# Optimization experiments

Measured on AMD Instinct MI355X. Metric: run time of the kernel, lower is better.

## Reference

```python
import jax, jax.numpy as jnp
import numpy as np

DIM = 768
HEADS = 12
HIDDEN = 4 * DIM
B, N = 8, 1024
EPS = 1e-5


def setup_inputs() -> dict:
    key = jax.random.key(0)
    ks = jax.random.split(key, 8)
    s = 0.02
    return {
        "x": jax.random.normal(ks[0], (B, N, DIM), dtype=jnp.float32),
        "ln1_g": jnp.ones((DIM,), jnp.float32),
        "ln1_b": jnp.zeros((DIM,), jnp.float32),
        "qkv_w": jax.random.normal(ks[1], (3 * DIM, DIM), jnp.float32) * s,
        "proj_w": jax.random.normal(ks[2], (DIM, DIM), jnp.float32) * s,
        "proj_b": jnp.zeros((DIM,), jnp.float32),
        "ln2_g": jnp.ones((DIM,), jnp.float32),
        "ln2_b": jnp.zeros((DIM,), jnp.float32),
        "fc1_w": jax.random.normal(ks[3], (HIDDEN, DIM), jnp.float32) * s,
        "fc1_b": jnp.zeros((HIDDEN,), jnp.float32),
        "fc2_w": jax.random.normal(ks[4], (DIM, HIDDEN), jnp.float32) * s,
        "fc2_b": jnp.zeros((DIM,), jnp.float32),
    }


def _layernorm(x, g, b):
    mu = jnp.mean(x, axis=-1, keepdims=True)
    var = jnp.mean(jnp.square(x - mu), axis=-1, keepdims=True)
    return (x - mu) * jax.lax.rsqrt(var + EPS) * g + b


def reference(x, ln1_g, ln1_b, qkv_w, proj_w, proj_b, ln2_g, ln2_b, fc1_w, fc1_b, fc2_w, fc2_b):
    Bn, Nn, C = x.shape
    H = HEADS
    D = C // H
    scale = D ** -0.5

    # --- attention branch ---
    h = _layernorm(x, ln1_g, ln1_b)
    qkv = h @ qkv_w.T                      # [B,N,3C] (qkv_bias=False)
    qkv = qkv.reshape(Bn, Nn, 3, H, D)
    q = qkv[:, :, 0].transpose(0, 2, 1, 3)  # [B,H,N,D]
    k = qkv[:, :, 1].transpose(0, 2, 1, 3)
    v = qkv[:, :, 2].transpose(0, 2, 1, 3)
    attn = jnp.einsum('bhnd,bhmd->bhnm', q, k) * scale  # [B,H,N,N]
    attn = jax.nn.softmax(attn, axis=-1)
    ctx = jnp.einsum('bhnm,bhmd->bhnd', attn, v)         # [B,H,N,D]
    ctx = ctx.transpose(0, 2, 1, 3).reshape(Bn, Nn, C)
    x = x + ctx @ proj_w.T + proj_b

    # --- MLP branch ---
    h = _layernorm(x, ln2_g, ln2_b)
    h = jax.nn.gelu(h @ fc1_w.T + fc1_b, approximate=False)
    return x + h @ fc2_w.T + fc2_b
```

## Files before the change

kernel.cpp:

```cpp
#include <hip/hip_runtime.h>
#include <cstdint>

typedef __attribute__((ext_vector_type(8))) short short8;
typedef __attribute__((ext_vector_type(4))) float f32x4;
typedef unsigned short u16t;

__device__ __forceinline__ u16t f2bf(float f) {
  uint32_t u = __float_as_uint(f);
  u += 0x7fffu + ((u >> 16) & 1u);
  return (u16t)(u >> 16);
}

__device__ __forceinline__ void gload_lds16(const void* g, void* l) {
  __builtin_amdgcn_global_load_lds(
      (const __attribute__((address_space(1))) void*)g,
      (__attribute__((address_space(3))) void*)l, 16, 0, 0);
}

__global__ __launch_bounds__(256) void cvt_bf16_kernel(const float* __restrict__ in,
                                                       u16t* __restrict__ out, int n8) {
  int i = blockIdx.x * 256 + threadIdx.x;
  if (i >= n8) return;
  const float4* p = (const float4*)in + (size_t)i * 2;
  float4 a = p[0], b = p[1];
  union { short8 v; u16t e[8]; } r;
  r.e[0] = f2bf(a.x); r.e[1] = f2bf(a.y); r.e[2] = f2bf(a.z); r.e[3] = f2bf(a.w);
  r.e[4] = f2bf(b.x); r.e[5] = f2bf(b.y); r.e[6] = f2bf(b.z); r.e[7] = f2bf(b.w);
  *((short8*)out + i) = r.v;
}

__global__ __launch_bounds__(256) void ln_kernel(const float* __restrict__ x,
                                                 const float* __restrict__ g,
                                                 const float* __restrict__ b,
                                                 u16t* __restrict__ out) {
  int row = blockIdx.x, tid = threadIdx.x;
  int wave = tid >> 6, lane = tid & 63;
  const float* xr = x + (size_t)row * 768;
  float v0 = xr[tid], v1 = xr[tid + 256], v2 = xr[tid + 512];
  float s = v0 + v1 + v2;
  float q = v0 * v0 + v1 * v1 + v2 * v2;
#pragma unroll
  for (int m = 32; m >= 1; m >>= 1) {
    s += __shfl_xor(s, m, 64);
    q += __shfl_xor(q, m, 64);
  }
  __shared__ float red[8];
  if (lane == 0) { red[wave] = s; red[4 + wave] = q; }
  __syncthreads();
  s = red[0] + red[1] + red[2] + red[3];
  q = red[4] + red[5] + red[6] + red[7];
  float mu = s * (1.0f / 768.0f);
  float var = q * (1.0f / 768.0f) - mu * mu;
  float rs = rsqrtf(var + 1e-5f);
  u16t* orow = out + (size_t)row * 768;
  orow[tid]       = f2bf((v0 - mu) * rs * g[tid]       + b[tid]);
  orow[tid + 256] = f2bf((v1 - mu) * rs * g[tid + 256] + b[tid + 256]);
  orow[tid + 512] = f2bf((v2 - mu) * rs * g[tid + 512] + b[tid + 512]);
}

template <int EPI, int BM>
__global__ __launch_bounds__(256, 2) void gemm_bt(const u16t* __restrict__ A,
                                                  const u16t* __restrict__ W,
                                                  void* __restrict__ Cout,
                                                  const float* __restrict__ bias,
                                                  const float* __restrict__ res,
                                                  int M, int N, int K) {
  __shared__ __align__(16) u16t As[BM * 64];
  __shared__ __align__(16) u16t Bs[128 * 64];
  constexpr int MF = BM / 32;
  int tid = threadIdx.x;
  int wave = tid >> 6, lane = tid & 63;
  int wr = wave >> 1, wc = wave & 1;
  int bm = blockIdx.y * BM;
  int bn = blockIdx.x * 128;
  f32x4 acc[MF][4] = {};

  int lr = lane >> 3;
  int lc = lane & 7;
  int srcslot = lc ^ lr;
  const u16t* Abase = A + (size_t)(bm + lr) * K + srcslot * 8;
  const u16t* Wbase = W + (size_t)(bn + lr) * K + srcslot * 8;

  for (int kt = 0; kt < K; kt += 64) {
    __syncthreads();
#pragma unroll
    for (int i = 0; i < BM / 32; i++) {
      int chunk = wave * (BM / 32) + i;
      gload_lds16(Abase + (size_t)(chunk * 8) * K + kt, (void*)(As + chunk * 512));
    }
#pragma unroll
    for (int i = 0; i < 4; i++) {
      int chunk = wave * 4 + i;
      gload_lds16(Wbase + (size_t)(chunk * 8) * K + kt, (void*)(Bs + chunk * 512));
    }
    __syncthreads();

    short8 af[MF][2], bfr[4][2];
#pragma unroll
    for (int m = 0; m < MF; m++) {
      int row = wr * (BM / 2) + m * 16 + (lane & 15);
#pragma unroll
      for (int s = 0; s < 2; s++) {
        int slot = s * 4 + (lane >> 4);
        af[m][s] = *(const short8*)(As + row * 64 + ((slot ^ (row & 7)) * 8));
      }
    }
#pragma unroll
    for (int n = 0; n < 4; n++) {
      int row = wc * 64 + n * 16 + (lane & 15);
#pragma unroll
      for (int s = 0; s < 2; s++) {
        int slot = s * 4 + (lane >> 4);
        bfr[n][s] = *(const short8*)(Bs + row * 64 + ((slot ^ (row & 7)) * 8));
      }
    }
    __builtin_amdgcn_s_setprio(1);
#pragma unroll
    for (int m = 0; m < MF; m++)
#pragma unroll
      for (int n = 0; n < 4; n++) {
        acc[m][n] = __builtin_amdgcn_mfma_f32_16x16x32_bf16(af[m][0], bfr[n][0], acc[m][n], 0, 0, 0);
        acc[m][n] = __builtin_amdgcn_mfma_f32_16x16x32_bf16(af[m][1], bfr[n][1], acc[m][n], 0, 0, 0);
      }
    __builtin_amdgcn_s_setprio(0);
  }

#pragma unroll
  for (int m = 0; m < MF; m++) {
#pragma unroll
    for (int n = 0; n < 4; n++) {
      int r0 = bm + wr * (BM / 2) + m * 16 + (lane >> 4) * 4;
      int c = bn + wc * 64 + n * 16 + (lane & 15);
#pragma unroll
      for (int i = 0; i < 4; i++) {
        int r = r0 + i;
        float v = acc[m][n][i];
        if constexpr (EPI == 0) {
          ((u16t*)Cout)[(size_t)r * N + c] = f2bf(v);
        } else if constexpr (EPI == 1) {
          ((float*)Cout)[(size_t)r * N + c] = v + bias[c] + res[(size_t)r * N + c];
        } else {
          v += bias[c];
          float gl = 0.5f * v * (1.0f + erff(v * 0.70710678118f));
          ((u16t*)Cout)[(size_t)r * N + c] = f2bf(gl);
        }
      }
    }
  }
}

__global__ __launch_bounds__(256, 2) void attn_kernel(const u16t* __restrict__ qkv,
                                                      u16t* __restrict__ ctx) {
  __shared__ __align__(16) u16t Ks[2][64 * 64];
  __shared__ __align__(16) u16t Vt[2][64 * 72];
  __shared__ __align__(16) u16t Ps[4][16 * 72];
  int tid = threadIdx.x;
  int wave = tid >> 6, lane = tid & 63;
  int b = blockIdx.x / 12, h = blockIdx.x % 12;
  int qt = blockIdx.y * 64;
  const u16t* base = qkv + (size_t)b * 1024 * 2304 + h * 64;

  int qrow = qt + wave * 16 + (lane & 15);
  const u16t* qp = base + (size_t)qrow * 2304 + (lane >> 4) * 8;
  short8 aq0 = *(const short8*)qp;
  short8 aq1 = *(const short8*)(qp + 32);

  const u16t* kbase = base + 768;
  const u16t* vbase = base + 1536;
  int lr = lane >> 3, lc = lane & 7;
  const u16t* kst = kbase + (size_t)lr * 2304 + ((lc ^ lr) * 8);
  const u16t* vst = vbase + (size_t)lane * 2304 + wave * 16;

  float m_i[4] = {-1e30f, -1e30f, -1e30f, -1e30f};
  float l_i[4] = {0.f, 0.f, 0.f, 0.f};
  f32x4 o[4] = {};
  const float scale = 0.125f;
  u16t* Pw = Ps[wave];

  union { uint4 u; u16t e[8]; } v0u, v1u;

  auto loadV = [&](int kt) {
    const u16t* vp = vst + (size_t)kt * 2304;
    v0u.u = *(const uint4*)vp;
    v1u.u = *(const uint4*)(vp + 8);
  };
  auto stageK = [&](int kt, int buf) {
#pragma unroll
    for (int i = 0; i < 2; i++) {
      int chunk = wave * 2 + i;
      gload_lds16(kst + (size_t)(kt + chunk * 8) * 2304, (void*)(Ks[buf] + chunk * 512));
    }
  };
  auto writeV = [&](int buf) {
#pragma unroll
    for (int j = 0; j < 8; j++) Vt[buf][(wave * 16 + j) * 72 + lane] = v0u.e[j];
#pragma unroll
    for (int j = 0; j < 8; j++) Vt[buf][(wave * 16 + 8 + j) * 72 + lane] = v1u.e[j];
  };

  loadV(0);
  stageK(0, 0);
  writeV(0);
  __syncthreads();

  for (int t = 0; t < 16; ++t) {
    int buf = t & 1;
    if (t < 15) {
      loadV((t + 1) * 64);
      stageK((t + 1) * 64, buf ^ 1);
    }

    const u16t* Kb = Ks[buf];
    f32x4 s[4] = {};
    __builtin_amdgcn_s_setprio(1);
#pragma unroll
    for (int n = 0; n < 4; n++) {
      int row = n * 16 + (lane & 15);
      int s0 = (lane >> 4);
      short8 bk0 = *(const short8*)(Kb + row * 64 + ((s0 ^ (row & 7)) * 8));
      short8 bk1 = *(const short8*)(Kb + row * 64 + (((s0 + 4) ^ (row & 7)) * 8));
      s[n] = __builtin_amdgcn_mfma_f32_16x16x32_bf16(aq0, bk0, s[n], 0, 0, 0);
      s[n] = __builtin_amdgcn_mfma_f32_16x16x32_bf16(aq1, bk1, s[n], 0, 0, 0);
    }
    __builtin_amdgcn_s_setprio(0);

    float alpha[4];
#pragma unroll
    for (int i = 0; i < 4; i++) {
      float mt = fmaxf(fmaxf(s[0][i], s[1][i]), fmaxf(s[2][i], s[3][i]));
      mt = fmaxf(mt, __shfl_xor(mt, 1, 64));
      mt = fmaxf(mt, __shfl_xor(mt, 2, 64));
      mt = fmaxf(mt, __shfl_xor(mt, 4, 64));
      mt = fmaxf(mt, __shfl_xor(mt, 8, 64));
      float mnew = fmaxf(m_i[i], mt * scale);
      alpha[i] = __expf(m_i[i] - mnew);
      m_i[i] = mnew;
    }
    float rsum[4] = {0.f, 0.f, 0.f, 0.f};
#pragma unroll
    for (int n = 0; n < 4; n++)
#pragma unroll
      for (int i = 0; i < 4; i++) {
        float p = __expf(s[n][i] * scale - m_i[i]);
        s[n][i] = p;
        rsum[i] += p;
      }
#pragma unroll
    for (int i = 0; i < 4; i++) {
      rsum[i] += __shfl_xor(rsum[i], 1, 64);
      rsum[i] += __shfl_xor(rsum[i], 2, 64);
      rsum[i] += __shfl_xor(rsum[i], 4, 64);
      rsum[i] += __shfl_xor(rsum[i], 8, 64);
      l_i[i] = l_i[i] * alpha[i] + rsum[i];
    }
#pragma unroll
    for (int n = 0; n < 4; n++)
#pragma unroll
      for (int i = 0; i < 4; i++)
        Pw[((lane >> 4) * 4 + i) * 72 + n * 16 + (lane & 15)] = f2bf(s[n][i]);
#pragma unroll
    for (int nd = 0; nd < 4; nd++)
#pragma unroll
      for (int i = 0; i < 4; i++) o[nd][i] *= alpha[i];
    const u16t* Vb = Vt[buf];
    __builtin_amdgcn_s_setprio(1);
#pragma unroll
    for (int st = 0; st < 2; st++) {
      short8 ap = *(const short8*)(Pw + (lane & 15) * 72 + st * 32 + (lane >> 4) * 8);
#pragma unroll
      for (int nd = 0; nd < 4; nd++) {
        short8 bv = *(const short8*)(Vb + (nd * 16 + (lane & 15)) * 72 + st * 32 + (lane >> 4) * 8);
        o[nd] = __builtin_amdgcn_mfma_f32_16x16x32_bf16(ap, bv, o[nd], 0, 0, 0);
      }
    }
    __builtin_amdgcn_s_setprio(0);

    if (t < 15) writeV(buf ^ 1);
    __syncthreads();
  }

#pragma unroll
  for (int i = 0; i < 4; i++) l_i[i] = 1.0f / l_i[i];
  int q0 = qt + wave * 16 + (lane >> 4) * 4;
#pragma unroll
  for (int i = 0; i < 4; i++) {
    u16t* crow = ctx + (size_t)(b * 1024 + q0 + i) * 768 + h * 64;
#pragma unroll
    for (int nd = 0; nd < 4; nd++)
      crow[nd * 16 + (lane & 15)] = f2bf(o[nd][i] * l_i[i]);
  }
}

extern "C" void kernel_launch(void* const* d_in, const int* in_sizes, int n_in,
                              void* d_out, int out_size, void* d_ws, size_t ws_size,
                              hipStream_t stream) {
  const float* x      = (const float*)d_in[0];
  const float* ln1_g  = (const float*)d_in[1];
  const float* ln1_b  = (const float*)d_in[2];
  const float* qkv_w  = (const float*)d_in[3];
  const float* proj_w = (const float*)d_in[4];
  const float* proj_b = (const float*)d_in[5];
  const float* ln2_g  = (const float*)d_in[6];
  const float* ln2_b  = (const float*)d_in[7];
  const float* fc1_w  = (const float*)d_in[8];
  const float* fc1_b  = (const float*)d_in[9];
  const float* fc2_w  = (const float*)d_in[10];
  const float* fc2_b  = (const float*)d_in[11];

  char* ws = (char*)d_ws;
  u16t* h1   = (u16t*)(ws + 0);
  u16t* qkvb = (u16t*)(ws + 12582912);
  u16t* ctx  = (u16t*)(ws + 50331648);
  float* x2  = (float*)(ws + 62914560);
  u16t* hid  = (u16t*)(ws + 88080384);
  u16t* wq   = (u16t*)(ws + 138412032);
  u16t* wp   = (u16t*)(ws + 141950976);
  u16t* w1   = (u16t*)(ws + 143130624);
  u16t* w2   = (u16t*)(ws + 147849216);
  float* out = (float*)d_out;

  cvt_bf16_kernel<<<864, 256, 0, stream>>>(qkv_w, wq, 221184);
  cvt_bf16_kernel<<<288, 256, 0, stream>>>(proj_w, wp, 73728);
  cvt_bf16_kernel<<<1152, 256, 0, stream>>>(fc1_w, w1, 294912);
  cvt_bf16_kernel<<<1152, 256, 0, stream>>>(fc2_w, w2, 294912);

  ln_kernel<<<8192, 256, 0, stream>>>(x, ln1_g, ln1_b, h1);
  gemm_bt<0, 128><<<dim3(18, 64), 256, 0, stream>>>(h1, wq, qkvb, nullptr, nullptr, 8192, 2304, 768);
  attn_kernel<<<dim3(96, 16), 256, 0, stream>>>(qkvb, ctx);
  gemm_bt<1, 64><<<dim3(6, 128), 256, 0, stream>>>(ctx, wp, x2, proj_b, x, 8192, 768, 768);
  ln_kernel<<<8192, 256, 0, stream>>>(x2, ln2_g, ln2_b, h1);
  gemm_bt<2, 128><<<dim3(24, 64), 256, 0, stream>>>(h1, w1, hid, fc1_b, nullptr, 8192, 3072, 768);
  gemm_bt<1, 64><<<dim3(6, 128), 256, 0, stream>>>(hid, w2, out, fc2_b, x2, 8192, 768, 3072);
}
```

Baseline: 305.9 us.

## Pre-transpose V and restructure attention to load K/V fragments from global

```diff
diff --git a/kernel.cpp b/kernel.cpp
--- a/kernel.cpp
+++ b/kernel.cpp
@@ -9,6 +9,12 @@
   uint32_t u = __float_as_uint(f);
   u += 0x7fffu + ((u >> 16) & 1u);
   return (u16t)(u >> 16);
+}
+
+__device__ __forceinline__ uint32_t cvtpk(float lo, float hi) {
+  uint32_t r;
+  asm("v_cvt_pk_bf16_f32 %0, %1, %2" : "=v"(r) : "v"(lo), "v"(hi));
+  return r;
 }
 
 __device__ __forceinline__ void gload_lds16(const void* g, void* l) {
@@ -149,145 +155,182 @@
   }
 }
 
-__global__ __launch_bounds__(256, 2) void attn_kernel(const u16t* __restrict__ qkv,
+__global__ __launch_bounds__(256) void vtrans_kernel(const u16t* __restrict__ qkv,
+                                                     u16t* __restrict__ vt) {
+  __shared__ u16t T[64][66];
+  int h = blockIdx.x % 12, bb = blockIdx.x / 12, kt = blockIdx.y * 64;
+  int t = threadIdx.x;
+  int r = t >> 2, dc = t & 3;
+  const u16t* src = qkv + (size_t)(bb * 1024 + kt + r) * 2304 + 1536 + h * 64 + dc * 16;
+  union { uint4 u[2]; u16t e[16]; uint32_t w[8]; } buf;
+  buf.u[0] = *(const uint4*)src;
+  buf.u[1] = *(const uint4*)(src + 8);
+#pragma unroll
+  for (int j = 0; j < 8; j++)
+    *(uint32_t*)&T[r][dc * 16 + 2 * j] = buf.w[j];
+  __syncthreads();
+  int d = t >> 2, kc = t & 3;
+  union { uint4 u[2]; u16t e[16]; } o;
+#pragma unroll
+  for (int j = 0; j < 16; j++) o.e[j] = T[kc * 16 + j][d];
+  u16t* dst = vt + ((size_t)blockIdx.x * 64 + d) * 1024 + kt + kc * 16;
+  *(uint4*)dst = o.u[0];
+  *(uint4*)(dst + 8) = o.u[1];
+}
+
+__global__ __launch_bounds__(256, 3) void attn_kernel(const u16t* __restrict__ qkv,
+                                                      const u16t* __restrict__ vt,
                                                       u16t* __restrict__ ctx) {
-  __shared__ __align__(16) u16t Ks[2][64 * 64];
-  __shared__ __align__(16) u16t Vt[2][64 * 72];
-  __shared__ __align__(16) u16t Ps[4][16 * 72];
+  __shared__ __align__(16) u16t Plds[4][32 * 72];
   int tid = threadIdx.x;
   int wave = tid >> 6, lane = tid & 63;
-  int b = blockIdx.x / 12, h = blockIdx.x % 12;
-  int qt = blockIdx.y * 64;
+  int q = lane & 15, g = lane >> 4;
+
+  int bid = blockIdx.x;
+  int xcd = bid & 7, j = bid >> 3;
+  int head = xcd + 8 * (j >> 3);
+  int qt = (j & 7) * 128 + wave * 32;
+  int b = head / 12, h = head % 12;
+
   const u16t* base = qkv + (size_t)b * 1024 * 2304 + h * 64;
-
-  int qrow = qt + wave * 16 + (lane & 15);
-  const u16t* qp = base + (size_t)qrow * 2304 + (lane >> 4) * 8;
-  short8 aq0 = *(const short8*)qp;
-  short8 aq1 = *(const short8*)(qp + 32);
-
   const u16t* kbase = base + 768;
-  const u16t* vbase = base + 1536;
-  int lr = lane >> 3, lc = lane & 7;
-  const u16t* kst = kbase + (size_t)lr * 2304 + ((lc ^ lr) * 8);
-  const u16t* vst = vbase + (size_t)lane * 2304 + wave * 16;
-
-  float m_i[4] = {-1e30f, -1e30f, -1e30f, -1e30f};
-  float l_i[4] = {0.f, 0.f, 0.f, 0.f};
-  f32x4 o[4] = {};
-  const float scale = 0.125f;
-  u16t* Pw = Ps[wave];
-
-  union { uint4 u; u16t e[8]; } v0u, v1u;
-
-  auto loadV = [&](int kt) {
-    const u16t* vp = vst + (size_t)kt * 2304;
-    v0u.u = *(const uint4*)vp;
-    v1u.u = *(const uint4*)(vp + 8);
-  };
-  auto stageK = [&](int kt, int buf) {
-#pragma unroll
-    for (int i = 0; i < 2; i++) {
-      int chunk = wave * 2 + i;
-      gload_lds16(kst + (size_t)(kt + chunk * 8) * 2304, (void*)(Ks[buf] + chunk * 512));
-    }
-  };
-  auto writeV = [&](int buf) {
-#pragma unroll
-    for (int j = 0; j < 8; j++) Vt[buf][(wave * 16 + j) * 72 + lane] = v0u.e[j];
-#pragma unroll
-    for (int j = 0; j < 8; j++) Vt[buf][(wave * 16 + 8 + j) * 72 + lane] = v1u.e[j];
-  };
-
-  loadV(0);
-  stageK(0, 0);
-  writeV(0);
-  __syncthreads();
-
-  for (int t = 0; t < 16; ++t) {
-    int buf = t & 1;
-    if (t < 15) {
-      loadV((t + 1) * 64);
-      stageK((t + 1) * 64, buf ^ 1);
-    }
-
-    const u16t* Kb = Ks[buf];
-    f32x4 s[4] = {};
+  const u16t* vtb = vt + (size_t)head * 64 * 1024;
+
+  short8 qf[2][2];
+#pragma unroll
+  for (int hf = 0; hf < 2; hf++)
+#pragma unroll
+    for (int hh = 0; hh < 2; hh++)
+      qf[hf][hh] = *(const short8*)(base + (size_t)(qt + hf * 16 + q) * 2304 + hh * 32 + g * 8);
+
+  float mA = -1e30f, mB = -1e30f, lA = 0.f, lB = 0.f;
+  f32x4 oA[4] = {}, oB[4] = {};
+  u16t* Pw = Plds[wave];
+
+  for (int kt = 0; kt < 1024; kt += 64) {
+    short8 kf[4][2], vf[4][2];
+#pragma unroll
+    for (int n = 0; n < 4; n++)
+#pragma unroll
+      for (int hh = 0; hh < 2; hh++)
+        kf[n][hh] = *(const short8*)(kbase + (size_t)(kt + n * 16 + q) * 2304 + hh * 32 + g * 8);
+#pragma unroll
+    for (int n = 0; n < 4; n++)
+#pragma unroll
+      for (int hh = 0; hh < 2; hh++)
+        vf[n][hh] = *(const short8*)(vtb + (size_t)(n * 16 + q) * 1024 + kt + hh * 32 + g * 8);
+
+    f32x4 sA[4] = {}, sB[4] = {};
     __builtin_amdgcn_s_setprio(1);
 #pragma unroll
     for (int n = 0; n < 4; n++) {
-      int row = n * 16 + (lane & 15);
-      int s0 = (lane >> 4);
-      short8 bk0 = *(const short8*)(Kb + row * 64 + ((s0 ^ (row & 7)) * 8));
-      short8 bk1 = *(const short8*)(Kb + row * 64 + (((s0 + 4) ^ (row & 7)) * 8));
-      s[n] = __builtin_amdgcn_mfma_f32_16x16x32_bf16(aq0, bk0, s[n], 0, 0, 0);
-      s[n] = __builtin_amdgcn_mfma_f32_16x16x32_bf16(aq1, bk1, s[n], 0, 0, 0);
+      sA[n] = __builtin_amdgcn_mfma_f32_16x16x32_bf16(kf[n][0], qf[0][0], sA[n], 0, 0, 0);
+      sA[n] = __builtin_amdgcn_mfma_f32_16x16x32_bf16(kf[n][1], qf[0][1], sA[n], 0, 0, 0);
+      sB[n] = __builtin_amdgcn_mfma_f32_16x16x32_bf16(kf[n][0], qf[1][0], sB[n], 0, 0, 0);
+      sB[n] = __builtin_amdgcn_mfma_f32_16x16x32_bf16(kf[n][1], qf[1][1], sB[n], 0, 0, 0);
     }
     __builtin_amdgcn_s_setprio(0);
 
-    float alpha[4];
-#pragma unroll
-    for (int i = 0; i < 4; i++) {
-      float mt = fmaxf(fmaxf(s[0][i], s[1][i]), fmaxf(s[2][i], s[3][i]));
-      mt = fmaxf(mt, __shfl_xor(mt, 1, 64));
-      mt = fmaxf(mt, __shfl_xor(mt, 2, 64));
-      mt = fmaxf(mt, __shfl_xor(mt, 4, 64));
-      mt = fmaxf(mt, __shfl_xor(mt, 8, 64));
-      float mnew = fmaxf(m_i[i], mt * scale);
-      alpha[i] = __expf(m_i[i] - mnew);
-      m_i[i] = mnew;
-    }
-    float rsum[4] = {0.f, 0.f, 0.f, 0.f};
+    float alphaA, alphaB;
+    {
+      float tm = sA[0][0];
+#pragma unroll
+      for (int n = 0; n < 4; n++)
+#pragma unroll
+        for (int i = 0; i < 4; i++) tm = fmaxf(tm, sA[n][i]);
+      tm = fmaxf(tm, __shfl_xor(tm, 16, 64));
+      tm = fmaxf(tm, __shfl_xor(tm, 32, 64));
+      float mnew = fmaxf(mA, tm);
+      alphaA = __expf((mA - mnew) * 0.125f);
+      mA = mnew;
+      float rs = 0.f;
+#pragma unroll
+      for (int n = 0; n < 4; n++)
+#pragma unroll
+        for (int i = 0; i < 4; i++) {
+          float p = __expf((sA[n][i] - mnew) * 0.125f);
+          sA[n][i] = p;
+          rs += p;
+        }
+      rs += __shfl_xor(rs, 16, 64);
+      rs += __shfl_xor(rs, 32, 64);
+      lA = lA * alphaA + rs;
+#pragma unroll
+      for (int n = 0; n < 4; n++) {
+        uint32_t w0 = cvtpk(sA[n][0], sA[n][1]);
+        uint32_t w1 = cvtpk(sA[n][2], sA[n][3]);
+        *(uint2*)(Pw + q * 72 + n * 16 + g * 4) = make_uint2(w0, w1);
+      }
+    }
+    {
+      float tm = sB[0][0];
+#pragma unroll
+      for (int n = 0; n < 4; n++)
+#pragma unroll
+        for (int i = 0; i < 4; i++) tm = fmaxf(tm, sB[n][i]);
+      tm = fmaxf(tm, __shfl_xor(tm, 16, 64));
+      tm = fmaxf(tm, __shfl_xor(tm, 32, 64));
+      float mnew = fmaxf(mB, tm);
+      alphaB = __expf((mB - mnew) * 0.125f);
+      mB = mnew;
+      float rs = 0.f;
+#pragma unroll
+      for (int n = 0; n < 4; n++)
+#pragma unroll
+        for (int i = 0; i < 4; i++) {
+          float p = __expf((sB[n][i] - mnew) * 0.125f);
+          sB[n][i] = p;
+          rs += p;
+        }
+      rs += __shfl_xor(rs, 16, 64);
+      rs += __shfl_xor(rs, 32, 64);
+      lB = lB * alphaB + rs;
+#pragma unroll
+      for (int n = 0; n < 4; n++) {
+        uint32_t w0 = cvtpk(sB[n][0], sB[n][1]);
+        uint32_t w1 = cvtpk(sB[n][2], sB[n][3]);
+        *(uint2*)(Pw + (16 + q) * 72 + n * 16 + g * 4) = make_uint2(w0, w1);
+      }
+    }
+
 #pragma unroll
     for (int n = 0; n < 4; n++)
 #pragma unroll
       for (int i = 0; i < 4; i++) {
-        float p = __expf(s[n][i] * scale - m_i[i]);
-        s[n][i] = p;
-        rsum[i] += p;
-      }
-#pragma unroll
-    for (int i = 0; i < 4; i++) {
-      rsum[i] += __shfl_xor(rsum[i], 1, 64);
-      rsum[i] += __shfl_xor(rsum[i], 2, 64);
-      rsum[i] += __shfl_xor(rsum[i], 4, 64);
-      rsum[i] += __shfl_xor(rsum[i], 8, 64);
-      l_i[i] = l_i[i] * alpha[i] + rsum[i];
-    }
+        oA[n][i] *= alphaA;
+        oB[n][i] *= alphaB;
+      }
+
+    short8 pA[2], pB[2];
+#pragma unroll
+    for (int hh = 0; hh < 2; hh++) {
+      pA[hh] = *(const short8*)(Pw + q * 72 + hh * 32 + g * 8);
+      pB[hh] = *(const short8*)(Pw + (16 + q) * 72 + hh * 32 + g * 8);
+    }
+    __builtin_amdgcn_s_setprio(1);
 #pragma unroll
     for (int n = 0; n < 4; n++)
 #pragma unroll
-      for (int i = 0; i < 4; i++)
-        Pw[((lane >> 4) * 4 + i) * 72 + n * 16 + (lane & 15)] = f2bf(s[n][i]);
-#pragma unroll
-    for (int nd = 0; nd < 4; nd++)
-#pragma unroll
-      for (int i = 0; i < 4; i++) o[nd][i] *= alpha[i];
-    const u16t* Vb = Vt[buf];
-    __builtin_amdgcn_s_setprio(1);
-#pragma unroll
-    for (int st = 0; st < 2; st++) {
-      short8 ap = *(const short8*)(Pw + (lane & 15) * 72 + st * 32 + (lane >> 4) * 8);
-#pragma unroll
-      for (int nd = 0; nd < 4; nd++) {
-        short8 bv = *(const short8*)(Vb + (nd * 16 + (lane & 15)) * 72 + st * 32 + (lane >> 4) * 8);
-        o[nd] = __builtin_amdgcn_mfma_f32_16x16x32_bf16(ap, bv, o[nd], 0, 0, 0);
-      }
-    }
+      for (int hh = 0; hh < 2; hh++) {
+        oA[n] = __builtin_amdgcn_mfma_f32_16x16x32_bf16(vf[n][hh], pA[hh], oA[n], 0, 0, 0);
+        oB[n] = __builtin_amdgcn_mfma_f32_16x16x32_bf16(vf[n][hh], pB[hh], oB[n], 0, 0, 0);
+      }
     __builtin_amdgcn_s_setprio(0);
-
-    if (t < 15) writeV(buf ^ 1);
-    __syncthreads();
-  }
-
-#pragma unroll
-  for (int i = 0; i < 4; i++) l_i[i] = 1.0f / l_i[i];
-  int q0 = qt + wave * 16 + (lane >> 4) * 4;
-#pragma unroll
-  for (int i = 0; i < 4; i++) {
-    u16t* crow = ctx + (size_t)(b * 1024 + q0 + i) * 768 + h * 64;
-#pragma unroll
-    for (int nd = 0; nd < 4; nd++)
-      crow[nd * 16 + (lane & 15)] = f2bf(o[nd][i] * l_i[i]);
+  }
+
+  float invA = 1.f / lA, invB = 1.f / lB;
+  u16t* crowA = ctx + (size_t)(b * 1024 + qt + q) * 768 + h * 64;
+  u16t* crowB = ctx + (size_t)(b * 1024 + qt + 16 + q) * 768 + h * 64;
+#pragma unroll
+  for (int n = 0; n < 4; n++) {
+    uint32_t a0 = (uint32_t)f2bf(oA[n][0] * invA) | ((uint32_t)f2bf(oA[n][1] * invA) << 16);
+    uint32_t a1 = (uint32_t)f2bf(oA[n][2] * invA) | ((uint32_t)f2bf(oA[n][3] * invA) << 16);
+    *(uint32_t*)(crowA + n * 16 + g * 4) = a0;
+    *(uint32_t*)(crowA + n * 16 + g * 4 + 2) = a1;
+    uint32_t b0 = (uint32_t)f2bf(oB[n][0] * invB) | ((uint32_t)f2bf(oB[n][1] * invB) << 16);
+    uint32_t b1 = (uint32_t)f2bf(oB[n][2] * invB) | ((uint32_t)f2bf(oB[n][3] * invB) << 16);
+    *(uint32_t*)(crowB + n * 16 + g * 4) = b0;
+    *(uint32_t*)(crowB + n * 16 + g * 4 + 2) = b1;
   }
 }
 
@@ -317,6 +360,7 @@
   u16t* wp   = (u16t*)(ws + 141950976);
   u16t* w1   = (u16t*)(ws + 143130624);
   u16t* w2   = (u16t*)(ws + 147849216);
+  u16t* vtb  = h1;
   float* out = (float*)d_out;
 
   cvt_bf16_kernel<<<864, 256, 0, stream>>>(qkv_w, wq, 221184);
@@ -326,7 +370,8 @@
 
   ln_kernel<<<8192, 256, 0, stream>>>(x, ln1_g, ln1_b, h1);
   gemm_bt<0, 128><<<dim3(18, 64), 256, 0, stream>>>(h1, wq, qkvb, nullptr, nullptr, 8192, 2304, 768);
-  attn_kernel<<<dim3(96, 16), 256, 0, stream>>>(qkvb, ctx);
+  vtrans_kernel<<<dim3(96, 16), 256, 0, stream>>>(qkvb, vtb);
+  attn_kernel<<<768, 256, 0, stream>>>(qkvb, vtb, ctx);
   gemm_bt<1, 64><<<dim3(6, 128), 256, 0, stream>>>(ctx, wp, x2, proj_b, x, 8192, 768, 768);
   ln_kernel<<<8192, 256, 0, stream>>>(x2, ln2_g, ln2_b, h1);
   gemm_bt<2, 128><<<dim3(24, 64), 256, 0, stream>>>(h1, w1, hid, fc1_b, nullptr, 8192, 3072, 768);
```

After: 306.5 us. No clear change (+0.2%).
